# Kernel optimization log

Hardware: AMD Instinct MI355X
Metric: run time of the kernel (lower is better)

Reference implementation:

```python
import jax, jax.numpy as jnp
import numpy as np

B, DIM1, DIM2, DIM3 = 4, 2048, 4096, 4096


def setup_inputs() -> dict:
    key = jax.random.key(0)
    k1, k2, k3 = jax.random.split(key, 3)
    x = jax.random.normal(k1, (B, DIM1, DIM2), dtype=jnp.float32)
    y = jax.random.normal(k2, (B, DIM1, DIM3), dtype=jnp.float32)
    weight = jax.random.normal(k3, (DIM2, DIM3), dtype=jnp.float32)
    return {"x": x, "y": y, "weight": weight}


def reference(x, y, weight):
    # Out = hardswish(mish(leaky_relu(x @ W, 0.01) + y)) + 0.5
    v = jnp.einsum('bik,kn->bin', x, weight)              # (B, dim1, dim3)
    v = jnp.where(v >= 0, v, 0.01 * v)                    # LeakyReLU(0.01)
    v = v + y
    v = v * jnp.tanh(jax.nn.softplus(v))                  # Mish
    relu6 = jnp.clip(v + 3.0, 0.0, 6.0)
    v = v * relu6 * (1.0 / 6.0) + 0.5                     # HardSwish + 0.5 (baked into kernel)
    return v
```

## Files before the change

### kernel.cpp

```cpp
#include <hip/hip_runtime.h>
#include <hip/hip_bf16.h>
#include <cstdint>

typedef __attribute__((ext_vector_type(8))) short short8;
typedef __attribute__((ext_vector_type(4))) float f32x4;
typedef unsigned short ushort_t;

#define MM 8192
#define NN 4096
#define KK 4096

#define BM 128
#define BN 128
#define BK 64
#define NT (KK / BK)

#define MFMA_BF16 __builtin_amdgcn_mfma_f32_16x16x32_bf16

__device__ __forceinline__ ushort_t f2bf(float f) {
  uint32_t u = __builtin_bit_cast(uint32_t, f);
  u = (u + 0x7FFFu + ((u >> 16) & 1u)) >> 16;
  return (ushort_t)u;
}

__device__ __forceinline__ float epilogue(float v, float yv) {
  v = fmaxf(v, 0.01f * v);
  v += yv;
  const float vc = fminf(v, 15.f);
  const float t = __builtin_amdgcn_exp2f(vc * 1.44269504f);
  const float d = t * t + 2.f * t;
  const float mi = v * d * __builtin_amdgcn_rcpf(d + 2.f);
  const float r6 = fminf(fmaxf(mi + 3.f, 0.f), 6.f);
  return mi * r6 * (1.f / 6.f) + 0.5f;
}

__device__ __forceinline__ void gload_lds16(const void* g, void* l) {
  __builtin_amdgcn_global_load_lds(
      (const __attribute__((address_space(1))) unsigned int*)g,
      (__attribute__((address_space(3))) unsigned int*)l, 16, 0, 0);
}

#define CVT_BLOCKS ((MM * KK) / (256 * 8))
#define WT_BLOCKS ((NN / 32) * (KK / 32))

template <int DO_X>
__global__ void prep_kernel(const float* __restrict__ X, ushort_t* __restrict__ XB,
                            const float* __restrict__ W, ushort_t* __restrict__ WT) {
  __shared__ float t[32][33];
  const int bid = blockIdx.x;
  const int tid = threadIdx.x;
  if (DO_X && bid < CVT_BLOCKS) {
    const size_t i = ((size_t)bid * 256 + tid) * 8;
    f32x4 v0 = __builtin_nontemporal_load(reinterpret_cast<const f32x4*>(&X[i]));
    f32x4 v1 = __builtin_nontemporal_load(reinterpret_cast<const f32x4*>(&X[i + 4]));
    short8 o;
    o[0] = (short)f2bf(v0[0]); o[1] = (short)f2bf(v0[1]);
    o[2] = (short)f2bf(v0[2]); o[3] = (short)f2bf(v0[3]);
    o[4] = (short)f2bf(v1[0]); o[5] = (short)f2bf(v1[1]);
    o[6] = (short)f2bf(v1[2]); o[7] = (short)f2bf(v1[3]);
    *reinterpret_cast<short8*>(&XB[i]) = o;
  } else {
    const int b2 = DO_X ? (bid - CVT_BLOCKS) : bid;
    const int n0 = (b2 & 127) * 32, k0 = (b2 >> 7) * 32;
    const int tx = tid & 31, ty = tid >> 5;
#pragma unroll
    for (int i = ty; i < 32; i += 8)
      t[i][tx] = __builtin_nontemporal_load(&W[(size_t)(k0 + i) * NN + n0 + tx]);
    __syncthreads();
#pragma unroll
    for (int i = ty; i < 32; i += 8)
      WT[(size_t)(n0 + i) * KK + k0 + tx] = f2bf(t[tx][i]);
  }
}

#define LDSE 32768

#define STAGE_A(buf, h, kt)                                                    \
  {                                                                            \
    const int r_ = (h) * 64 + wid * 8;                                         \
    gload_lds16(XB + offA[h][0] + (kt), &lds[(buf) * LDSE + r_ * 64]);         \
    gload_lds16(XB + offA[h][1] + (kt), &lds[(buf) * LDSE + (r_ + 128) * 64]); \
  }

#define STAGE_B(buf, qn, kt)                                                   \
  {                                                                            \
    const int r_ = (qn) * 32 + (wid >> 2) * 64 + (wid & 3) * 8;                \
    gload_lds16(WT + offB[qn][0] + (kt),                                       \
                &lds[(buf) * LDSE + 16384 + r_ * 64]);                         \
    gload_lds16(WT + offB[qn][1] + (kt),                                       \
                &lds[(buf) * LDSE + 16384 + (r_ + 128) * 64]);                 \
  }

#define LOAD_A(dst, buf, qm)                                                   \
  _Pragma("unroll") for (int i = 0; i < 4; ++i) {                              \
    dst[0][i] = *reinterpret_cast<const short8*>(                              \
        &lds[(buf) * LDSE + aOff + (qm) * 4096 + i * 1024 + slot0]);           \
    dst[1][i] = *reinterpret_cast<const short8*>(                              \
        &lds[(buf) * LDSE + aOff + (qm) * 4096 + i * 1024 + slot1]);           \
  }

#define LOAD_B(dst, buf, qn)                                                   \
  _Pragma("unroll") for (int jj = 0; jj < 2; ++jj) {                           \
    dst[0][jj] = *reinterpret_cast<const short8*>(                             \
        &lds[(buf) * LDSE + bOff + (qn) * 2048 + jj * 1024 + slot0]);          \
    dst[1][jj] = *reinterpret_cast<const short8*>(                             \
        &lds[(buf) * LDSE + bOff + (qn) * 2048 + jj * 1024 + slot1]);          \
  }

#define MFMA_QUAD(AF, BF, QM, QN)                                              \
  __builtin_amdgcn_s_setprio(1);                                               \
  _Pragma("unroll") for (int ks = 0; ks < 2; ++ks)                             \
      _Pragma("unroll") for (int i = 0; i < 4; ++i)                            \
          _Pragma("unroll") for (int jj = 0; jj < 2; ++jj)                     \
              acc[(QM) * 4 + i][(QN) * 2 + jj] =                               \
      MFMA_BF16(AF[ks][i], BF[ks][jj], acc[(QM) * 4 + i][(QN) * 2 + jj], 0, 0, 0); \
  __builtin_amdgcn_s_setprio(0);

#define BAR() __builtin_amdgcn_s_barrier()

#define TILE_BODY(cur, nxt, t)                                                 \
  {                                                                            \
    const int k1 = (((t) + 1) & (NT - 1)) * BK;                                \
    const int k2 = (((t) + 2) & (NT - 1)) * BK;                                \
                                  \
    LOAD_A(a, cur, 0);                                                         \
    LOAD_B(b, cur, 0);                                                         \
    STAGE_B(nxt, 0, k1);                                                       \
    BAR();                                                                     \
    MFMA_QUAD(a, b, 0, 0);                                                     \
    BAR();                                                                     \
                                  \
    LOAD_B(b, cur, 1);                                                         \
    STAGE_A(cur, 0, k2);                                                       \
    BAR();                                                                     \
    MFMA_QUAD(a, b, 0, 1);                                                     \
    BAR();                                                                     \
                                  \
    LOAD_A(a, cur, 1);                                                         \
    STAGE_B(cur, 1, k2);                                                       \
    BAR();                                                                     \
    MFMA_QUAD(a, b, 1, 1);                                                     \
    BAR();                                                                     \
                       \
    LOAD_B(b, cur, 0);                                                         \
    STAGE_A(cur, 1, k2);                                                       \
    asm volatile("s_waitcnt vmcnt(6)" ::: "memory");                           \
    BAR();                                                                     \
    MFMA_QUAD(a, b, 1, 0);                                                     \
    BAR();                                                                     \
  }

__global__ __launch_bounds__(512, 2) void gemm_bf16_256(
    const ushort_t* __restrict__ XB, const ushort_t* __restrict__ WT,
    const float* __restrict__ Y, float* __restrict__ O) {
  __shared__ ushort_t lds[2 * LDSE];

  const int wg = blockIdx.x;
  const int xcd = wg & 7;
  const int local = wg >> 3;
  const int bm0 = (local >> 1) * 256;
  const int bn0 = (xcd * 2 + (local & 1)) * 256;

  const int tid = threadIdx.x;
  const int lane = tid & 63;
  const int wid = tid >> 6;
  const int wmi = wid >> 2;
  const int wni = wid & 3;

  const int l8 = lane >> 3;
  const int sslot = (lane & 7) ^ l8;

  uint32_t offA[2][2], offB[2][2];
#pragma unroll
  for (int h = 0; h < 2; ++h)
#pragma unroll
    for (int q = 0; q < 2; ++q) {
      const int rA = h * 64 + wid * 8 + q * 128;
      offA[h][q] = (uint32_t)(bm0 + rA + l8) * KK + sslot * 8;
      const int rB = h * 32 + (wid >> 2) * 64 + (wid & 3) * 8 + q * 128;
      offB[h][q] = (uint32_t)(bn0 + rB + l8) * KK + sslot * 8;
    }

  const int lr = lane & 15, lg = lane >> 4, lr7 = lane & 7;
  const int slot0 = (lg ^ lr7) * 8;
  const int slot1 = ((4 | lg) ^ lr7) * 8;
  const int aOff = (wmi * 128 + lr) * 64;
  const int bOff = 16384 + (wni * 64 + lr) * 64;

  f32x4 acc[8][4] = {};
  short8 a[2][4], b[2][2];

  STAGE_A(0, 0, 0);
  STAGE_B(0, 0, 0);
  STAGE_B(0, 1, 0);
  STAGE_A(0, 1, 0);
  STAGE_A(1, 0, BK);
  STAGE_B(1, 1, BK);
  STAGE_A(1, 1, BK);
  asm volatile("s_waitcnt vmcnt(6)" ::: "memory");
  BAR();

#pragma unroll 1
  for (int t = 0; t < NT; t += 2) {
    TILE_BODY(0, 1, t);
    TILE_BODY(1, 0, t + 1);
  }

#pragma unroll
  for (int mi = 0; mi < 8; ++mi) {
#pragma unroll
    for (int nj = 0; nj < 4; ++nj) {
#pragma unroll
      for (int r = 0; r < 4; ++r) {
        const int grow = bm0 + wmi * 128 + mi * 16 + lg * 4 + r;
        const int gcol = bn0 + wni * 64 + nj * 16 + lr;
        const size_t idx = (size_t)grow * NN + gcol;
        const float yv = __builtin_nontemporal_load(&Y[idx]);
        __builtin_nontemporal_store(epilogue(acc[mi][nj][r], yv), &O[idx]);
      }
    }
  }
}

#define LDP 72
__global__ __launch_bounds__(256, 3) void gemm_fused(
    const float* __restrict__ X, const ushort_t* __restrict__ WT,
    const float* __restrict__ Y, float* __restrict__ O) {
  __shared__ ushort_t Asm[BM * LDP];
  __shared__ ushort_t Bsm[BN * LDP];

  const int nwg = (MM / BM) * (NN / BN);
  int wg = blockIdx.x;
  wg = (wg % 8) * (nwg / 8) + wg / 8;
  const int NTC = NN / BN;
  const int bm0 = (wg / NTC) * BM;
  const int bn0 = (wg % NTC) * BN;

  const int tid = threadIdx.x;
  const int lane = tid & 63;
  const int wid = tid >> 6;
  const int wm = (wid >> 1) * 64, wn = (wid & 1) * 64;
  const int lr = lane & 15, lg = lane >> 4;

  f32x4 acc[4][4] = {};

  const int arow = tid >> 2;
  const int ac = (tid & 3) * 4;
  const int brow = tid >> 1;
  const int bc0 = (tid & 1) * 32;

  for (int kt = 0; kt < KK; kt += BK) {
    __syncthreads();
#pragma unroll
    for (int p = 0; p < 2; ++p) {
      const int row = arow + p * 64;
      const float* src = &X[(size_t)(bm0 + row) * KK + kt];
#pragma unroll
      for (int j = 0; j < 4; ++j) {
        f32x4 v = *reinterpret_cast<const f32x4*>(&src[ac + j * 16]);
        uint2 packed;
        packed.x = (uint32_t)f2bf(v[0]) | ((uint32_t)f2bf(v[1]) << 16);
        packed.y = (uint32_t)f2bf(v[2]) | ((uint32_t)f2bf(v[3]) << 16);
        *reinterpret_cast<uint2*>(&Asm[row * LDP + ac + j * 16]) = packed;
      }
    }
    {
      const ushort_t* src = &WT[(size_t)(bn0 + brow) * KK + kt + bc0];
#pragma unroll
      for (int j = 0; j < 4; ++j) {
        short8 u = *reinterpret_cast<const short8*>(&src[j * 8]);
        *reinterpret_cast<short8*>(&Bsm[brow * LDP + bc0 + j * 8]) = u;
      }
    }
    __syncthreads();

#pragma unroll
    for (int ks = 0; ks < 2; ++ks) {
      short8 a[4], b[4];
#pragma unroll
      for (int i = 0; i < 4; ++i) {
        a[i] = *reinterpret_cast<const short8*>(&Asm[(wm + i * 16 + lr) * LDP + ks * 32 + lg * 8]);
        b[i] = *reinterpret_cast<const short8*>(&Bsm[(wn + i * 16 + lr) * LDP + ks * 32 + lg * 8]);
      }
#pragma unroll
      for (int i = 0; i < 4; ++i)
#pragma unroll
        for (int j = 0; j < 4; ++j)
          acc[i][j] = MFMA_BF16(a[i], b[j], acc[i][j], 0, 0, 0);
    }
  }

#pragma unroll
  for (int i = 0; i < 4; ++i) {
#pragma unroll
    for (int j = 0; j < 4; ++j) {
#pragma unroll
      for (int r = 0; r < 4; ++r) {
        const int grow = bm0 + wm + i * 16 + lg * 4 + r;
        const int gcol = bn0 + wn + j * 16 + lr;
        const size_t idx = (size_t)grow * NN + gcol;
        O[idx] = epilogue(acc[i][j][r], Y[idx]);
      }
    }
  }
}

__global__ void naive_fused(const float* __restrict__ X, const float* __restrict__ W,
                            const float* __restrict__ Y, float* __restrict__ O) {
  const int n0 = (blockIdx.x * 256 + threadIdx.x) * 4;
  const int m = blockIdx.y;
  f32x4 acc = {0.f, 0.f, 0.f, 0.f};
  const float* xr = &X[(size_t)m * KK];
  for (int k = 0; k < KK; ++k) {
    const float xv = xr[k];
    const f32x4 wv = *reinterpret_cast<const f32x4*>(&W[(size_t)k * NN + n0]);
    acc[0] += xv * wv[0];
    acc[1] += xv * wv[1];
    acc[2] += xv * wv[2];
    acc[3] += xv * wv[3];
  }
  const size_t idx = (size_t)m * NN + n0;
  O[idx + 0] = epilogue(acc[0], Y[idx + 0]);
  O[idx + 1] = epilogue(acc[1], Y[idx + 1]);
  O[idx + 2] = epilogue(acc[2], Y[idx + 2]);
  O[idx + 3] = epilogue(acc[3], Y[idx + 3]);
}

extern "C" void kernel_launch(void* const* d_in, const int* in_sizes, int n_in,
                              void* d_out, int out_size, void* d_ws, size_t ws_size,
                              hipStream_t stream) {
  const float* x = (const float*)d_in[0];
  const float* y = (const float*)d_in[1];
  const float* w = (const float*)d_in[2];
  float* out = (float*)d_out;

  const size_t xb_bytes = (size_t)MM * KK * sizeof(ushort_t);
  const size_t wt_bytes = (size_t)NN * KK * sizeof(ushort_t);

  if (ws_size >= xb_bytes + wt_bytes) {
    ushort_t* XB = (ushort_t*)d_ws;
    ushort_t* WT = (ushort_t*)((char*)d_ws + xb_bytes);
    hipLaunchKernelGGL((prep_kernel<1>), dim3(CVT_BLOCKS + WT_BLOCKS), dim3(256), 0, stream,
                       x, XB, w, WT);
    hipLaunchKernelGGL(gemm_bf16_256, dim3((MM / 256) * (NN / 256)), dim3(512), 0, stream,
                       XB, WT, y, out);
  } else if (ws_size >= wt_bytes) {
    ushort_t* WT = (ushort_t*)d_ws;
    hipLaunchKernelGGL((prep_kernel<0>), dim3(WT_BLOCKS), dim3(256), 0, stream,
                       x, nullptr, w, WT);
    hipLaunchKernelGGL(gemm_fused, dim3((MM / BM) * (NN / BN)), dim3(256), 0, stream,
                       x, WT, y, out);
  } else {
    hipLaunchKernelGGL(naive_fused, dim3(NN / 1024, MM), dim3(256), 0, stream, x, w, y, out);
  }
}
```

Before: 329.0 us.

## Fuse X fp32-to-bf16 conversion into GEMM A-tile staging via registers

Removes the separate pass that converts X to bf16 in workspace. The GEMM now loads fp32 X tiles into registers a stage ahead, converts them with packed bf16 cvt instructions, and writes them to LDS in place of the direct global-to-LDS loads. The goal is to cut the extra read and write of the X matrix, at the cost of more registers, VALU work and LDS stores in the main loop, plus twice the bytes per A load from global memory. The older 128-tile fused fallback kernel is deleted.

```diff
diff --git a/kernel.cpp b/kernel.cpp
--- a/kernel.cpp
+++ b/kernel.cpp
@@ -40,7 +40,6 @@
       (__attribute__((address_space(3))) unsigned int*)l, 16, 0, 0);
 }
 
-#define CVT_BLOCKS ((MM * KK) / (256 * 8))
 #define WT_BLOCKS ((NN / 32) * (KK / 32))
 
 template <int DO_X>
@@ -49,38 +48,18 @@
   __shared__ float t[32][33];
   const int bid = blockIdx.x;
   const int tid = threadIdx.x;
-  if (DO_X && bid < CVT_BLOCKS) {
-    const size_t i = ((size_t)bid * 256 + tid) * 8;
-    f32x4 v0 = __builtin_nontemporal_load(reinterpret_cast<const f32x4*>(&X[i]));
-    f32x4 v1 = __builtin_nontemporal_load(reinterpret_cast<const f32x4*>(&X[i + 4]));
-    short8 o;
-    o[0] = (short)f2bf(v0[0]); o[1] = (short)f2bf(v0[1]);
-    o[2] = (short)f2bf(v0[2]); o[3] = (short)f2bf(v0[3]);
-    o[4] = (short)f2bf(v1[0]); o[5] = (short)f2bf(v1[1]);
-    o[6] = (short)f2bf(v1[2]); o[7] = (short)f2bf(v1[3]);
-    *reinterpret_cast<short8*>(&XB[i]) = o;
-  } else {
-    const int b2 = DO_X ? (bid - CVT_BLOCKS) : bid;
-    const int n0 = (b2 & 127) * 32, k0 = (b2 >> 7) * 32;
-    const int tx = tid & 31, ty = tid >> 5;
-#pragma unroll
-    for (int i = ty; i < 32; i += 8)
-      t[i][tx] = __builtin_nontemporal_load(&W[(size_t)(k0 + i) * NN + n0 + tx]);
-    __syncthreads();
-#pragma unroll
-    for (int i = ty; i < 32; i += 8)
-      WT[(size_t)(n0 + i) * KK + k0 + tx] = f2bf(t[tx][i]);
-  }
+  const int n0 = (bid & 127) * 32, k0 = (bid >> 7) * 32;
+  const int tx = tid & 31, ty = tid >> 5;
+#pragma unroll
+  for (int i = ty; i < 32; i += 8)
+    t[i][tx] = __builtin_nontemporal_load(&W[(size_t)(k0 + i) * NN + n0 + tx]);
+  __syncthreads();
+#pragma unroll
+  for (int i = ty; i < 32; i += 8)
+    WT[(size_t)(n0 + i) * KK + k0 + tx] = f2bf(t[tx][i]);
 }
 
 #define LDSE 32768
-
-#define STAGE_A(buf, h, kt)                                                    \
-  {                                                                            \
-    const int r_ = (h) * 64 + wid * 8;                                         \
-    gload_lds16(XB + offA[h][0] + (kt), &lds[(buf) * LDSE + r_ * 64]);         \
-    gload_lds16(XB + offA[h][1] + (kt), &lds[(buf) * LDSE + (r_ + 128) * 64]); \
-  }
 
 #define STAGE_B(buf, qn, kt)                                                   \
   {                                                                            \
@@ -89,6 +68,29 @@
                 &lds[(buf) * LDSE + 16384 + r_ * 64]);                         \
     gload_lds16(WT + offB[qn][1] + (kt),                                       \
                 &lds[(buf) * LDSE + 16384 + (r_ + 128) * 64]);                 \
+  }
+
+#define LDA_F32(dst, h, kv)                                                    \
+  _Pragma("unroll") for (int q = 0; q < 2; ++q) {                              \
+    dst[q * 2 + 0] = *reinterpret_cast<const f32x4*>(X + xA[h][q] + (kv));     \
+    dst[q * 2 + 1] = *reinterpret_cast<const f32x4*>(X + xA[h][q] + (kv) + 4); \
+  }
+
+#define WRA(buf, h, src)                                                       \
+  _Pragma("unroll") for (int q = 0; q < 2; ++q) {                              \
+    uint32_t d0, d1, d2, d3;                                                   \
+    asm("v_cvt_pk_bf16_f32 %0, %1, %2"                                         \
+        : "=v"(d0) : "v"(src[q * 2][0]), "v"(src[q * 2][1]));                  \
+    asm("v_cvt_pk_bf16_f32 %0, %1, %2"                                         \
+        : "=v"(d1) : "v"(src[q * 2][2]), "v"(src[q * 2][3]));                  \
+    asm("v_cvt_pk_bf16_f32 %0, %1, %2"                                         \
+        : "=v"(d2) : "v"(src[q * 2 + 1][0]), "v"(src[q * 2 + 1][1]));          \
+    asm("v_cvt_pk_bf16_f32 %0, %1, %2"                                         \
+        : "=v"(d3) : "v"(src[q * 2 + 1][2]), "v"(src[q * 2 + 1][3]));          \
+    uint4 w_; w_.x = d0; w_.y = d1; w_.z = d2; w_.w = d3;                      \
+    *reinterpret_cast<uint4*>(                                                 \
+        &lds[(buf) * LDSE +                                                    \
+             ((h) * 64 + wid * 8 + q * 128 + l8) * 64 + (lane & 7) * 8]) = w_; \
   }
 
 #define LOAD_A(dst, buf, qm)                                                   \
@@ -122,36 +124,39 @@
   {                                                                            \
     const int k1 = (((t) + 1) & (NT - 1)) * BK;                                \
     const int k2 = (((t) + 2) & (NT - 1)) * BK;                                \
-                                  \
+    const int k3 = (((t) + 3) & (NT - 1)) * BK;                                \
+                       \
     LOAD_A(a, cur, 0);                                                         \
     LOAD_B(b, cur, 0);                                                         \
+    LDA_F32(fA1, 1, k2);                                                       \
     STAGE_B(nxt, 0, k1);                                                       \
     BAR();                                                                     \
     MFMA_QUAD(a, b, 0, 0);                                                     \
     BAR();                                                                     \
-                                  \
+               \
     LOAD_B(b, cur, 1);                                                         \
-    STAGE_A(cur, 0, k2);                                                       \
+    WRA(cur, 0, fA0);                                                          \
     BAR();                                                                     \
     MFMA_QUAD(a, b, 0, 1);                                                     \
     BAR();                                                                     \
-                                  \
+                       \
     LOAD_A(a, cur, 1);                                                         \
+    LDA_F32(fA0, 0, k3);                                                       \
     STAGE_B(cur, 1, k2);                                                       \
     BAR();                                                                     \
     MFMA_QUAD(a, b, 1, 1);                                                     \
     BAR();                                                                     \
-                       \
+            \
     LOAD_B(b, cur, 0);                                                         \
-    STAGE_A(cur, 1, k2);                                                       \
+    WRA(cur, 1, fA1);                                                          \
     asm volatile("s_waitcnt vmcnt(6)" ::: "memory");                           \
     BAR();                                                                     \
     MFMA_QUAD(a, b, 1, 0);                                                     \
     BAR();                                                                     \
   }
 
-__global__ __launch_bounds__(512, 2) void gemm_bf16_256(
-    const ushort_t* __restrict__ XB, const ushort_t* __restrict__ WT,
+__global__ __launch_bounds__(512, 2) void gemm_bf16_f(
+    const float* __restrict__ X, const ushort_t* __restrict__ WT,
     const float* __restrict__ Y, float* __restrict__ O) {
   __shared__ ushort_t lds[2 * LDSE];
 
@@ -170,13 +175,19 @@
   const int l8 = lane >> 3;
   const int sslot = (lane & 7) ^ l8;
 
-  uint32_t offA[2][2], offB[2][2];
+  uint32_t xA[2][2];
 #pragma unroll
   for (int h = 0; h < 2; ++h)
 #pragma unroll
     for (int q = 0; q < 2; ++q) {
       const int rA = h * 64 + wid * 8 + q * 128;
-      offA[h][q] = (uint32_t)(bm0 + rA + l8) * KK + sslot * 8;
+      xA[h][q] = (uint32_t)(bm0 + rA + l8) * KK + sslot * 8;
+    }
+  uint32_t offB[2][2];
+#pragma unroll
+  for (int h = 0; h < 2; ++h)
+#pragma unroll
+    for (int q = 0; q < 2; ++q) {
       const int rB = h * 32 + (wid >> 2) * 64 + (wid & 3) * 8 + q * 128;
       offB[h][q] = (uint32_t)(bn0 + rB + l8) * KK + sslot * 8;
     }
@@ -189,15 +200,18 @@
 
   f32x4 acc[8][4] = {};
   short8 a[2][4], b[2][2];
-
-  STAGE_A(0, 0, 0);
+  f32x4 fA0[4], fA1[4];
+
+  LDA_F32(fA0, 0, 0);  WRA(0, 0, fA0);
+  LDA_F32(fA0, 1, 0);  WRA(0, 1, fA0);
+  LDA_F32(fA0, 0, BK); WRA(1, 0, fA0);
+  LDA_F32(fA0, 1, BK); WRA(1, 1, fA0);
   STAGE_B(0, 0, 0);
   STAGE_B(0, 1, 0);
-  STAGE_A(0, 1, 0);
-  STAGE_A(1, 0, BK);
   STAGE_B(1, 1, BK);
-  STAGE_A(1, 1, BK);
+  LDA_F32(fA0, 0, 2 * BK);
   asm volatile("s_waitcnt vmcnt(6)" ::: "memory");
+  asm volatile("s_waitcnt lgkmcnt(0)");
   BAR();
 
 #pragma unroll 1
@@ -217,89 +231,6 @@
         const size_t idx = (size_t)grow * NN + gcol;
         const float yv = __builtin_nontemporal_load(&Y[idx]);
         __builtin_nontemporal_store(epilogue(acc[mi][nj][r], yv), &O[idx]);
-      }
-    }
-  }
-}
-
-#define LDP 72
-__global__ __launch_bounds__(256, 3) void gemm_fused(
-    const float* __restrict__ X, const ushort_t* __restrict__ WT,
-    const float* __restrict__ Y, float* __restrict__ O) {
-  __shared__ ushort_t Asm[BM * LDP];
-  __shared__ ushort_t Bsm[BN * LDP];
-
-  const int nwg = (MM / BM) * (NN / BN);
-  int wg = blockIdx.x;
-  wg = (wg % 8) * (nwg / 8) + wg / 8;
-  const int NTC = NN / BN;
-  const int bm0 = (wg / NTC) * BM;
-  const int bn0 = (wg % NTC) * BN;
-
-  const int tid = threadIdx.x;
-  const int lane = tid & 63;
-  const int wid = tid >> 6;
-  const int wm = (wid >> 1) * 64, wn = (wid & 1) * 64;
-  const int lr = lane & 15, lg = lane >> 4;
-
-  f32x4 acc[4][4] = {};
-
-  const int arow = tid >> 2;
-  const int ac = (tid & 3) * 4;
-  const int brow = tid >> 1;
-  const int bc0 = (tid & 1) * 32;
-
-  for (int kt = 0; kt < KK; kt += BK) {
-    __syncthreads();
-#pragma unroll
-    for (int p = 0; p < 2; ++p) {
-      const int row = arow + p * 64;
-      const float* src = &X[(size_t)(bm0 + row) * KK + kt];
-#pragma unroll
-      for (int j = 0; j < 4; ++j) {
-        f32x4 v = *reinterpret_cast<const f32x4*>(&src[ac + j * 16]);
-        uint2 packed;
-        packed.x = (uint32_t)f2bf(v[0]) | ((uint32_t)f2bf(v[1]) << 16);
-        packed.y = (uint32_t)f2bf(v[2]) | ((uint32_t)f2bf(v[3]) << 16);
-        *reinterpret_cast<uint2*>(&Asm[row * LDP + ac + j * 16]) = packed;
-      }
-    }
-    {
-      const ushort_t* src = &WT[(size_t)(bn0 + brow) * KK + kt + bc0];
-#pragma unroll
-      for (int j = 0; j < 4; ++j) {
-        short8 u = *reinterpret_cast<const short8*>(&src[j * 8]);
-        *reinterpret_cast<short8*>(&Bsm[brow * LDP + bc0 + j * 8]) = u;
-      }
-    }
-    __syncthreads();
-
-#pragma unroll
-    for (int ks = 0; ks < 2; ++ks) {
-      short8 a[4], b[4];
-#pragma unroll
-      for (int i = 0; i < 4; ++i) {
-        a[i] = *reinterpret_cast<const short8*>(&Asm[(wm + i * 16 + lr) * LDP + ks * 32 + lg * 8]);
-        b[i] = *reinterpret_cast<const short8*>(&Bsm[(wn + i * 16 + lr) * LDP + ks * 32 + lg * 8]);
-      }
-#pragma unroll
-      for (int i = 0; i < 4; ++i)
-#pragma unroll
-        for (int j = 0; j < 4; ++j)
-          acc[i][j] = MFMA_BF16(a[i], b[j], acc[i][j], 0, 0, 0);
-    }
-  }
-
-#pragma unroll
-  for (int i = 0; i < 4; ++i) {
-#pragma unroll
-    for (int j = 0; j < 4; ++j) {
-#pragma unroll
-      for (int r = 0; r < 4; ++r) {
-        const int grow = bm0 + wm + i * 16 + lg * 4 + r;
-        const int gcol = bn0 + wn + j * 16 + lr;
-        const size_t idx = (size_t)grow * NN + gcol;
-        O[idx] = epilogue(acc[i][j][r], Y[idx]);
       }
     }
   }
@@ -334,21 +265,13 @@
   const float* w = (const float*)d_in[2];
   float* out = (float*)d_out;
 
-  const size_t xb_bytes = (size_t)MM * KK * sizeof(ushort_t);
   const size_t wt_bytes = (size_t)NN * KK * sizeof(ushort_t);
 
-  if (ws_size >= xb_bytes + wt_bytes) {
-    ushort_t* XB = (ushort_t*)d_ws;
-    ushort_t* WT = (ushort_t*)((char*)d_ws + xb_bytes);
-    hipLaunchKernelGGL((prep_kernel<1>), dim3(CVT_BLOCKS + WT_BLOCKS), dim3(256), 0, stream,
-                       x, XB, w, WT);
-    hipLaunchKernelGGL(gemm_bf16_256, dim3((MM / 256) * (NN / 256)), dim3(512), 0, stream,
-                       XB, WT, y, out);
-  } else if (ws_size >= wt_bytes) {
+  if (ws_size >= wt_bytes) {
     ushort_t* WT = (ushort_t*)d_ws;
     hipLaunchKernelGGL((prep_kernel<0>), dim3(WT_BLOCKS), dim3(256), 0, stream,
                        x, nullptr, w, WT);
-    hipLaunchKernelGGL(gemm_fused, dim3((MM / BM) * (NN / BN)), dim3(256), 0, stream,
+    hipLaunchKernelGGL(gemm_bf16_f, dim3((MM / 256) * (NN / 256)), dim3(512), 0, stream,
                        x, WT, y, out);
   } else {
     hipLaunchKernelGGL(naive_fused, dim3(NN / 1024, MM), dim3(256), 0, stream, x, w, y, out);
```

After: 520.8 us. 1.58x slower.
